# Kernel tuning notes

Measured on AMD Instinct MI355X. Metric: run time of the kernel, lower is better.

## Reference

```python
import jax, jax.numpy as jnp
import numpy as np

B, H, W, C = 2, 256, 256, 192
HEADS, WS, SHIFT = 6, 8, 4
N = WS * WS              # tokens per window = 64
NW = (H // WS) * (W // WS)  # windows per image = 1024
DH = C // HEADS
HID = 4 * C
EPS = 1e-5


def _rel_pos_index(ws):
    coords = np.stack(np.meshgrid(np.arange(ws), np.arange(ws), indexing='ij'))  # (2, ws, ws)
    flat = coords.reshape(2, -1)
    rel = flat[:, :, None] - flat[:, None, :]           # (2, N, N)
    rel = rel.transpose(1, 2, 0).astype(np.int64)       # (N, N, 2)
    rel[:, :, 0] += ws - 1
    rel[:, :, 1] += ws - 1
    rel[:, :, 0] *= 2 * ws - 1
    return rel.sum(-1).astype(np.int32)                 # (N, N)


def _attn_mask(h, w, ws, shift):
    img = np.zeros((h, w), np.float32)
    slc = (slice(0, -ws), slice(-ws, -shift), slice(-shift, None))
    cnt = 0
    for hs in slc:
        for wcol in slc:
            img[hs, wcol] = cnt
            cnt += 1
    mw = img.reshape(h // ws, ws, w // ws, ws).transpose(0, 2, 1, 3).reshape(-1, ws * ws)
    am = mw[:, None, :] - mw[:, :, None]
    return np.where(am != 0, np.float32(-100.0), np.float32(0.0)).astype(np.float32)


def setup_inputs() -> dict:
    key = jax.random.key(0)
    ks = jax.random.split(key, 8)
    s = 0.02
    return {
        'x': jax.random.normal(ks[0], (B, H * W, C), jnp.float32),
        'ln1_g': jnp.ones((C,), jnp.float32),
        'ln1_b': jnp.zeros((C,), jnp.float32),
        'qkv_w': jax.random.normal(ks[1], (3 * C, C), jnp.float32) * s,
        'qkv_b': jnp.zeros((3 * C,), jnp.float32),
        'rpb_table': jax.random.normal(ks[2], ((2 * WS - 1) ** 2, HEADS), jnp.float32) * s,
        'proj_w': jax.random.normal(ks[3], (C, C), jnp.float32) * s,
        'proj_b': jnp.zeros((C,), jnp.float32),
        'ln2_g': jnp.ones((C,), jnp.float32),
        'ln2_b': jnp.zeros((C,), jnp.float32),
        'fc1_w': jax.random.normal(ks[4], (HID, C), jnp.float32) * s,
        'fc1_b': jnp.zeros((HID,), jnp.float32),
        'fc2_w': jax.random.normal(ks[5], (C, HID), jnp.float32) * s,
        'fc2_b': jnp.zeros((C,), jnp.float32),
        'attn_mask': jnp.asarray(_attn_mask(H, W, WS, SHIFT)),   # (NW, N, N)
        'rel_idx': jnp.asarray(_rel_pos_index(WS)),               # (N, N) int32
    }


def _ln(x, g, b):
    m = jnp.mean(x, axis=-1, keepdims=True)
    v = jnp.mean(jnp.square(x - m), axis=-1, keepdims=True)
    return (x - m) * jax.lax.rsqrt(v + EPS) * g + b


def reference(x, ln1_g, ln1_b, qkv_w, qkv_b, rpb_table, proj_w, proj_b,
              ln2_g, ln2_b, fc1_w, fc1_b, fc2_w, fc2_b, attn_mask, rel_idx):
    nH, nW = H // WS, W // WS
    shortcut = x
    h = _ln(x, ln1_g, ln1_b).reshape(B, H, W, C)
    # cyclic shift
    h = jnp.roll(h, (-SHIFT, -SHIFT), axis=(1, 2))
    # window partition -> (B*NW, N, C)
    wins = h.reshape(B, nH, WS, nW, WS, C).transpose(0, 1, 3, 2, 4, 5).reshape(B * NW, N, C)
    qkv = wins @ qkv_w.T + qkv_b                       # (B*NW, N, 3C)
    qkv = qkv.reshape(B * NW, N, 3, HEADS, DH).transpose(2, 0, 3, 1, 4)
    q, k, v = qkv[0], qkv[1], qkv[2]                   # (B*NW, heads, N, DH)
    scale = DH ** -0.5
    attn = jnp.einsum('bhnd,bhmd->bhnm', q * scale, k)  # (B*NW, heads, N, N)
    bias = rpb_table[rel_idx.reshape(-1)].reshape(N, N, HEADS).transpose(2, 0, 1)
    attn = attn + bias[None]
    # shifted-window mask: per-window additive mask
    attn = attn.reshape(B, NW, HEADS, N, N) + attn_mask[None, :, None]
    attn = jax.nn.softmax(attn, axis=-1).reshape(B * NW, HEADS, N, N)
    out = jnp.einsum('bhnm,bhmd->bhnd', attn, v)        # (B*NW, heads, N, DH)
    out = out.transpose(0, 2, 1, 3).reshape(B * NW, N, C)
    out = out @ proj_w.T + proj_b
    # window reverse + unshift
    out = out.reshape(B, nH, nW, WS, WS, C).transpose(0, 1, 3, 2, 4, 5).reshape(B, H, W, C)
    out = jnp.roll(out, (SHIFT, SHIFT), axis=(1, 2)).reshape(B, H * W, C)
    x = shortcut + out
    h2 = _ln(x, ln2_g, ln2_b)
    h2 = jax.nn.gelu(h2 @ fc1_w.T + fc1_b, approximate=False)
    return x + (h2 @ fc2_w.T + fc2_b)
```

## Files before the change

kernel.cpp:

```cpp
#include <hip/hip_runtime.h>
#include <hip/hip_bf16.h>
#include <math.h>

using bf16 = __hip_bfloat16;
typedef short bfrag __attribute__((ext_vector_type(8)));
typedef float f32x4 __attribute__((ext_vector_type(4)));

__device__ __forceinline__ float b2f(bf16 v){ return __bfloat162float(v); }
__device__ __forceinline__ bf16  f2b(float v){ return __float2bfloat16(v); }
__device__ __forceinline__ short f2bs(float v){ bf16 t = f2b(v); union{bf16 h; short s;} u; u.h = t; return u.s; }
__device__ __forceinline__ float bits2f(unsigned short s){ union{unsigned u; float f;} c; c.u = ((unsigned)s) << 16; return c.f; }
__device__ __forceinline__ int   pk2(float lo, float hi){
  return (((int)(unsigned short)f2bs(hi)) << 16) | (int)(unsigned short)f2bs(lo);
}
__device__ __forceinline__ float ldT(const float* p, long long i){ return p[i]; }
__device__ __forceinline__ float ldT(const bf16*  p, long long i){ return __bfloat162float(p[i]); }

__device__ __forceinline__ bfrag ldfrag(const bf16* p){ return *reinterpret_cast<const bfrag*>(p); }
__device__ __forceinline__ f32x4 mm16(bfrag a, bfrag b, f32x4 c){
  return __builtin_amdgcn_mfma_f32_16x16x32_bf16(a, b, c, 0, 0, 0);
}
__device__ __forceinline__ void gload_lds16(const void* g, void* l){
  __builtin_amdgcn_global_load_lds(
    (const __attribute__((address_space(1))) unsigned int*)g,
    (__attribute__((address_space(3))) unsigned int*)l, 16, 0, 0);
}

template<int CTRL>
__device__ __forceinline__ float dppf(float v){
  union{float f; int i;} u; u.f = v;
  u.i = __builtin_amdgcn_update_dpp(0, u.i, CTRL, 0xF, 0xF, true);
  return u.f;
}
__device__ __forceinline__ float rmax16(float v){
  v = fmaxf(v, dppf<0xB1>(v));  v = fmaxf(v, dppf<0x4E>(v));
  v = fmaxf(v, dppf<0x141>(v)); v = fmaxf(v, dppf<0x140>(v));
  return v;
}
__device__ __forceinline__ float rsum16(float v){
  v += dppf<0xB1>(v);  v += dppf<0x4E>(v);
  v += dppf<0x141>(v); v += dppf<0x140>(v);
  return v;
}
__device__ __forceinline__ float rsum4(float v){
  v += dppf<0xB1>(v); v += dppf<0x4E>(v);
  return v;
}

__device__ __forceinline__ int reg1(int g){ return (g >= 248) + (g >= 252); }
__device__ __forceinline__ long long natidx(int gw, int t){
  const int wl = gw & 1023;
  const int sr = (((wl >> 5) << 3) + (t >> 3) + 4) & 255;
  const int sc = (((wl & 31) << 3) + (t & 7) + 4) & 255;
  return (((long long)(gw >> 10)) << 16) + sr*256 + sc;
}

template<typename T>
__device__ __forceinline__ void ld48(const T* p, long long off, float* d){
  if constexpr (sizeof(T) == 4){
    #pragma unroll
    for (int i = 0; i < 12; ++i){
      float4 v = *reinterpret_cast<const float4*>((const float*)p + off + i*4);
      d[i*4+0]=v.x; d[i*4+1]=v.y; d[i*4+2]=v.z; d[i*4+3]=v.w;
    }
  } else {
    #pragma unroll
    for (int i = 0; i < 6; ++i){
      bfrag v = *reinterpret_cast<const bfrag*>((const bf16*)p + off + i*8);
      #pragma unroll
      for (int j = 0; j < 8; ++j) d[i*8+j] = bits2f((unsigned short)v[j]);
    }
  }
}

#define WS_QKV   0
#define WS_PROJ  221184
#define WS_FC1   294912
#define WS_FC2   589824
#define WS_BIAS6 884736

__global__ __launch_bounds__(256) void prep_k(const void* det,
    const void* qkvw, const void* projw, const void* fc1w, const void* fc2w,
    const void* rpb, const int* __restrict__ relidx, char* wsb)
{
  const bool isbf = (((const unsigned short*)det)[0] == 0x3F80u);
  const int gt = blockIdx.x * 256 + threadIdx.x;
  if (gt < 55296) {
    const int fid = gt >> 6, l = gt & 63;
    int f, nkt, ckw; const void* src; bf16* dst;
    if (fid < 216)      { f = fid;       nkt = 6;  ckw = 192; src = qkvw;  dst = (bf16*)(wsb + WS_QKV); }
    else if (fid < 288) { f = fid - 216; nkt = 6;  ckw = 192; src = projw; dst = (bf16*)(wsb + WS_PROJ); }
    else if (fid < 576) { f = fid - 288; nkt = 6;  ckw = 192; src = fc1w;  dst = (bf16*)(wsb + WS_FC1); }
    else                { f = fid - 576; nkt = 24; ckw = 768; src = fc2w;  dst = (bf16*)(wsb + WS_FC2); }
    const int ct = f / nkt, kt = f - ct * nkt;
    const long long ro = (long long)(ct*16 + (l & 15)) * ckw + kt*32 + (l >> 4)*8;
    bf16* dp = dst + ((long long)f * 64 + l) * 8;
    #pragma unroll
    for (int j = 0; j < 8; ++j) {
      float v = isbf ? b2f(((const bf16*)src)[ro + j]) : ((const float*)src)[ro + j];
      dp[j] = f2b(v);
    }
  } else if (gt < 55296 + 24576) {
    const int t = gt - 55296;
    const int h = t >> 12, ij = t & 4095;
    const int ri = relidx[ij];
    float v = isbf ? b2f(((const bf16*)rpb)[ri*6 + h]) : ((const float*)rpb)[ri*6 + h];
    ((float*)(wsb + WS_BIAS6))[t] = v;
  }
}

#define XN_S 200
#define QK_S 72
#define VT_S 72
#define LDS_K1 (64*XN_S*2 + 64*QK_S*2 + 32*VT_S*2)

template<typename T>
__device__ void attn_body(const T* __restrict__ x, const T* __restrict__ g1, const T* __restrict__ b1,
                          const bf16* __restrict__ qkvwp, const T* __restrict__ qkvb,
                          const bf16* __restrict__ projwp, const T* __restrict__ projb,
                          const float* __restrict__ bias6, char* __restrict__ dout,
                          int x2f32, char* smem)
{
  bf16* xn = (bf16*)smem;
  bf16* qk = xn + 64*XN_S;
  bf16* vt = qk + 64*QK_S;
  const int tid = threadIdx.x, l = tid & 63, w = tid >> 6;
  const int lr = l & 15, lg = l >> 4;
  const int gw = blockIdx.x;
  const int wl = gw & 1023, wi = wl >> 5, wj = wl & 31;

  {
    const int t = (w << 4) + (l >> 2);
    const int c0 = (l & 3) * 48;
    const long long base = natidx(gw, t) * 192 + c0;
    float xv[48];
    ld48(x, base, xv);
    float s1 = 0.f, s2 = 0.f;
    #pragma unroll
    for (int i = 0; i < 48; ++i){ s1 += xv[i]; s2 = fmaf(xv[i], xv[i], s2); }
    s1 = rsum4(s1); s2 = rsum4(s2);
    const float m  = s1 * (1.f/192.f);
    const float rs = rsqrtf(s2*(1.f/192.f) - m*m + 1e-5f);
    bf16* xr = xn + t*XN_S + c0;
    #pragma unroll
    for (int cb = 0; cb < 6; ++cb){
      bfrag o;
      #pragma unroll
      for (int j = 0; j < 8; ++j){
        const int c = cb*8 + j;
        o[j] = f2bs((xv[c]-m)*rs*ldT(g1, c0+c) + ldT(b1, c0+c));
      }
      *reinterpret_cast<bfrag*>(xr + cb*8) = o;
    }
  }
  __syncthreads();

  int rjh[4], rjw[4], rih[4], riw[4];
  #pragma unroll
  for (int ct = 0; ct < 4; ++ct){
    const int j = ct*16 + lr;
    rjh[ct] = reg1(wi*8 + (j >> 3));
    rjw[ct] = reg1(wj*8 + (j & 7));
  }
  #pragma unroll
  for (int r = 0; r < 4; ++r){
    const int i = w*16 + lg*4 + r;
    rih[r] = reg1(wi*8 + (i >> 3));
    riw[r] = reg1(wj*8 + (i & 7));
  }

  int ohpk[6][2][2];

  #pragma unroll
  for (int h = 0; h < 6; ++h){
    f32x4 acc[6];
    #pragma unroll
    for (int u = 0; u < 6; ++u) acc[u] = (f32x4){0.f,0.f,0.f,0.f};
    #pragma unroll
    for (int kt = 0; kt < 6; ++kt){
      bfrag a = ldfrag(&xn[(w*16 + lr)*XN_S + kt*32 + lg*8]);
      bfrag bq[6];
      #pragma unroll
      for (int u = 0; u < 6; ++u){
        const int ctg = (u >> 1)*12 + 2*h + (u & 1);
        bq[u] = ldfrag(qkvwp + ((long long)(ctg*6 + kt)*64 + l)*8);
      }
      #pragma unroll
      for (int u = 0; u < 6; ++u) acc[u] = mm16(a, bq[u], acc[u]);
    }
    __syncthreads();

    #pragma unroll
    for (int u = 0; u < 6; ++u){
      const int ctg = (u >> 1)*12 + 2*h + (u & 1);
      const float bia = ldT(qkvb, ctg*16 + lr);
      #pragma unroll
      for (int r = 0; r < 4; ++r){
        const int row = w*16 + lg*4 + r;
        const float v = acc[u][r] + bia;
        if (u < 2)      qk[row*QK_S + u*16 + lr] = f2b(v * 0.17677669529663687f);
        else if (u < 4) qk[row*QK_S + 32 + (u & 1)*16 + lr] = f2b(v);
        else            vt[((u & 1)*16 + lr)*VT_S + row] = f2b(v);
      }
    }
    __syncthreads();

    f32x4 s4[4];
    {
      bfrag aq = ldfrag(&qk[(w*16 + lr)*QK_S + lg*8]);
      #pragma unroll
      for (int ct = 0; ct < 4; ++ct)
        s4[ct] = mm16(aq, ldfrag(&qk[(ct*16 + lr)*QK_S + 32 + lg*8]), (f32x4){0.f,0.f,0.f,0.f});
    }
    const float* bh = bias6 + h*4096;
    float pr[4][4], inv4[4];
    #pragma unroll
    for (int r = 0; r < 4; ++r){
      const int i = w*16 + lg*4 + r;
      const int ib = i*64 + lr;
      float v[4];
      #pragma unroll
      for (int ct = 0; ct < 4; ++ct){
        const float msk = (rih[r] == rjh[ct] && riw[r] == rjw[ct]) ? 0.f : -100.f;
        v[ct] = s4[ct][r] + bh[ib + ct*16] + msk;
      }
      float mx = rmax16(fmaxf(fmaxf(v[0],v[1]), fmaxf(v[2],v[3])));
      v[0] = __expf(v[0]-mx); v[1] = __expf(v[1]-mx);
      v[2] = __expf(v[2]-mx); v[3] = __expf(v[3]-mx);
      const float sm = rsum16(v[0]+v[1]+v[2]+v[3]);
      inv4[r] = __fdividef(1.f, sm);
      pr[r][0]=v[0]; pr[r][1]=v[1]; pr[r][2]=v[2]; pr[r][3]=v[3];
    }
    __syncthreads();

    #pragma unroll
    for (int r = 0; r < 4; ++r){
      const int i = w*16 + lg*4 + r;
      #pragma unroll
      for (int ct = 0; ct < 4; ++ct)
        qk[i*QK_S + ct*16 + lr] = f2b(pr[r][ct]*inv4[r]);
    }
    f32x4 o2[2] = {(f32x4){0.f,0.f,0.f,0.f}, (f32x4){0.f,0.f,0.f,0.f}};
    #pragma unroll
    for (int ktp = 0; ktp < 2; ++ktp){
      bfrag ap = ldfrag(&qk[(w*16 + lr)*QK_S + ktp*32 + lg*8]);
      o2[0] = mm16(ap, ldfrag(&vt[(lr)*VT_S + ktp*32 + lg*8]), o2[0]);
      o2[1] = mm16(ap, ldfrag(&vt[(16 + lr)*VT_S + ktp*32 + lg*8]), o2[1]);
    }
    #pragma unroll
    for (int u = 0; u < 2; ++u){
      ohpk[h][u][0] = pk2(o2[u][0], o2[u][1]);
      ohpk[h][u][1] = pk2(o2[u][2], o2[u][3]);
    }
  }

  #pragma unroll
  for (int h = 0; h < 6; ++h)
    #pragma unroll
    for (int u = 0; u < 2; ++u)
      #pragma unroll
      for (int rr = 0; rr < 2; ++rr){
        const int pk = ohpk[h][u][rr];
        const int row = w*16 + lg*4 + rr*2;
        *reinterpret_cast<short*>(&xn[row*XN_S + h*32 + u*16 + lr]) = (short)(pk & 0xffff);
        *reinterpret_cast<short*>(&xn[(row+1)*XN_S + h*32 + u*16 + lr]) = (short)(((unsigned)pk) >> 16);
      }
  __syncthreads();

  const int mp = w >> 1, chh = w & 1;
  f32x4 pacc[2][6];
  #pragma unroll
  for (int mt = 0; mt < 2; ++mt)
    #pragma unroll
    for (int cc = 0; cc < 6; ++cc) pacc[mt][cc] = (f32x4){0.f,0.f,0.f,0.f};
  #pragma unroll
  for (int kt = 0; kt < 6; ++kt){
    bfrag a0 = ldfrag(&xn[(mp*32 + lr)*XN_S + kt*32 + lg*8]);
    bfrag a1 = ldfrag(&xn[(mp*32 + 16 + lr)*XN_S + kt*32 + lg*8]);
    #pragma unroll
    for (int cc = 0; cc < 6; ++cc){
      bfrag bp = ldfrag(projwp + ((long long)((chh*6 + cc)*6 + kt)*64 + l)*8);
      pacc[0][cc] = mm16(a0, bp, pacc[0][cc]);
      pacc[1][cc] = mm16(a1, bp, pacc[1][cc]);
    }
  }
  #pragma unroll
  for (int mt = 0; mt < 2; ++mt)
    #pragma unroll
    for (int r = 0; r < 4; ++r){
      const int t = mp*32 + mt*16 + lg*4 + r;
      const long long n = natidx(gw, t);
      #pragma unroll
      for (int cc = 0; cc < 6; ++cc){
        const int c = (chh*6 + cc)*16 + lr;
        const float y = pacc[mt][cc][r] + ldT(projb, c) + ldT(x, n*192 + c);
        if (x2f32) ((float*)(dout + n*768))[c] = y;
        else       ((bf16*)(dout + n*384))[c]  = f2b(y);
      }
    }
}

__global__ __launch_bounds__(256, 4) void swin_attn_k(
    const void* det, const void* x, const void* g1, const void* b1,
    const bf16* qkvwp, const void* qkvb, const bf16* projwp, const void* projb,
    const float* bias6, void* doutv)
{
  extern __shared__ char smem[];
  const bool isbf = (((const unsigned short*)det)[0] == 0x3F80u);
  char* dout = (char*)doutv;
  if (isbf)
    attn_body<bf16>((const bf16*)x, (const bf16*)g1, (const bf16*)b1, qkvwp,
                    (const bf16*)qkvb, projwp, (const bf16*)projb, bias6, dout, 0, smem);
  else
    attn_body<float>((const float*)x, (const float*)g1, (const float*)b1, qkvwp,
                     (const float*)qkvb, projwp, (const float*)projb, bias6, dout, 1, smem);
}

#define HS_S 72
#define LDS_K3 (48*512*2 + 128*HS_S*2)

template<typename T>
__device__ void mlp_body(const T* __restrict__ g2, const T* __restrict__ b2,
                         const bf16* __restrict__ fc1p, const T* __restrict__ fb1,
                         const bf16* __restrict__ fc2p, const T* __restrict__ fb2,
                         char* __restrict__ dout, int outf32, char* smem)
{
  bf16* xn2 = (bf16*)smem;
  bf16* bw  = (bf16*)smem;
  bf16* hs  = bw + 48*512;
  const int tid = threadIdx.x, l = tid & 63, w = tid >> 6;
  const int lr = l & 15, lg = l >> 4;
  const long long t0 = (long long)blockIdx.x * 128;

  #pragma unroll
  for (int it = 0; it < 2; ++it){
    const int t = w*32 + it*16 + (l >> 2);
    const int c0 = (l & 3) * 48;
    const long long n = t0 + t;
    float xv[48];
    if (outf32) ld48((const float*)(dout + n*768), c0, xv);
    else        ld48((const bf16*)(dout + n*384), c0, xv);
    float s1 = 0.f, s2 = 0.f;
    #pragma unroll
    for (int i = 0; i < 48; ++i){ s1 += xv[i]; s2 = fmaf(xv[i], xv[i], s2); }
    s1 = rsum4(s1); s2 = rsum4(s2);
    const float m  = s1 * (1.f/192.f);
    const float rs = rsqrtf(s2*(1.f/192.f) - m*m + 1e-5f);
    bf16* xr = xn2 + t*XN_S + c0;
    #pragma unroll
    for (int cb = 0; cb < 6; ++cb){
      bfrag o;
      #pragma unroll
      for (int j = 0; j < 8; ++j){
        const int c = cb*8 + j;
        o[j] = f2bs((xv[c]-m)*rs*ldT(g2, c0+c) + ldT(b2, c0+c));
      }
      *reinterpret_cast<bfrag*>(xr + cb*8) = o;
    }
  }
  __syncthreads();

  bfrag xa[2][6];
  #pragma unroll
  for (int mt = 0; mt < 2; ++mt)
    #pragma unroll
    for (int kt = 0; kt < 6; ++kt)
      xa[mt][kt] = ldfrag(&xn2[(w*32 + mt*16 + lr)*XN_S + kt*32 + lg*8]);
  __syncthreads();

  f32x4 fa[2][12];
  #pragma unroll
  for (int mt = 0; mt < 2; ++mt)
    #pragma unroll
    for (int ct = 0; ct < 12; ++ct) fa[mt][ct] = (f32x4){0.f,0.f,0.f,0.f};

  for (int c = 0; c < 12; ++c){
    {
      const int q0 = w*12;
      #pragma unroll
      for (int e = 0; e < 12; ++e){
        const int q = q0 + e;
        const bf16* src = (q < 24)
          ? fc1p + ((long long)(c*24 + q)*64 + l)*8
          : fc2p + ((long long)(((q-24) >> 1)*24 + c*2 + ((q-24) & 1))*64 + l)*8;
        gload_lds16(src, bw + q*512);
      }
    }
    __syncthreads();
    f32x4 a1[2][4];
    #pragma unroll
    for (int mt = 0; mt < 2; ++mt)
      #pragma unroll
      for (int u = 0; u < 4; ++u) a1[mt][u] = (f32x4){0.f,0.f,0.f,0.f};
    #pragma unroll
    for (int kt = 0; kt < 6; ++kt)
      #pragma unroll
      for (int u = 0; u < 4; ++u){
        bfrag bq = ldfrag(&bw[((u*6 + kt)*64 + l)*8]);
        a1[0][u] = mm16(xa[0][kt], bq, a1[0][u]);
        a1[1][u] = mm16(xa[1][kt], bq, a1[1][u]);
      }
    #pragma unroll
    for (int u = 0; u < 4; ++u){
      const float bia = ldT(fb1, c*64 + u*16 + lr);
      #pragma unroll
      for (int mt = 0; mt < 2; ++mt)
        #pragma unroll
        for (int r = 0; r < 4; ++r){
          const float xv = a1[mt][u][r] + bia;
          const float g  = __fdividef(xv, 1.f + __expf(-1.702f*xv));
          hs[(w*32 + mt*16 + lg*4 + r)*HS_S + u*16 + lr] = f2b(g);
        }
    }
    #pragma unroll
    for (int ktl = 0; ktl < 2; ++ktl){
      bfrag aH0 = ldfrag(&hs[(w*32 + lr)*HS_S + ktl*32 + lg*8]);
      bfrag aH1 = ldfrag(&hs[(w*32 + 16 + lr)*HS_S + ktl*32 + lg*8]);
      #pragma unroll
      for (int ct = 0; ct < 12; ++ct){
        bfrag bq = ldfrag(&bw[((24 + ct*2 + ktl)*64 + l)*8]);
        fa[0][ct] = mm16(aH0, bq, fa[0][ct]);
        fa[1][ct] = mm16(aH1, bq, fa[1][ct]);
      }
    }
    __syncthreads();
  }

  #pragma unroll
  for (int mt = 0; mt < 2; ++mt)
    #pragma unroll
    for (int r = 0; r < 4; ++r){
      const long long n = t0 + w*32 + mt*16 + lg*4 + r;
      #pragma unroll
      for (int ct = 0; ct < 12; ++ct){
        const int cc = ct*16 + lr;
        float resid = outf32 ? ((const float*)(dout + n*768))[cc]
                             : b2f(((const bf16*)(dout + n*384))[cc]);
        const float y = fa[mt][ct][r] + ldT(fb2, cc) + resid;
        if (outf32) ((float*)(dout + n*768))[cc] = y;
        else        ((bf16*)(dout + n*384))[cc]  = f2b(y);
      }
    }
}

__global__ __launch_bounds__(256, 2) void swin_mlp_k(
    const void* det, const void* g2, const void* b2, const bf16* fc1p, const void* fb1,
    const bf16* fc2p, const void* fb2, void* doutv)
{
  extern __shared__ char smem[];
  const bool isbf = (((const unsigned short*)det)[0] == 0x3F80u);
  char* dout = (char*)doutv;
  if (isbf)
    mlp_body<bf16>((const bf16*)g2, (const bf16*)b2, fc1p, (const bf16*)fb1,
                   fc2p, (const bf16*)fb2, dout, 0, smem);
  else
    mlp_body<float>((const float*)g2, (const float*)b2, fc1p, (const float*)fb1,
                    fc2p, (const float*)fb2, dout, 1, smem);
}

extern "C" void kernel_launch(void* const* d_in, const int* in_sizes, int n_in,
                              void* d_out, int out_size, void* d_ws, size_t ws_size,
                              hipStream_t stream)
{
  (void)in_sizes; (void)n_in; (void)out_size; (void)ws_size;
  char* ws = (char*)d_ws;

  (void)hipFuncSetAttribute((const void*)swin_attn_k, hipFuncAttributeMaxDynamicSharedMemorySize, LDS_K1);
  (void)hipFuncSetAttribute((const void*)swin_mlp_k,  hipFuncAttributeMaxDynamicSharedMemorySize, LDS_K3);

  prep_k<<<dim3(312), dim3(256), 0, stream>>>(
      d_in[1], d_in[3], d_in[6], d_in[10], d_in[12], d_in[5], (const int*)d_in[15], ws);

  swin_attn_k<<<dim3(2048), dim3(256), LDS_K1, stream>>>(
      d_in[1], d_in[0], d_in[1], d_in[2],
      (const bf16*)(ws + WS_QKV), d_in[4], (const bf16*)(ws + WS_PROJ), d_in[7],
      (const float*)(ws + WS_BIAS6), d_out);

  swin_mlp_k<<<dim3(1024), dim3(256), LDS_K3, stream>>>(
      d_in[1], d_in[8], d_in[9],
      (const bf16*)(ws + WS_FC1), d_in[11], (const bf16*)(ws + WS_FC2), d_in[13], d_out);
}
```

Measured before the change: 313.2 us.

## Hoist LN activations to registers and software-pipeline per-head QKV GEMM

The normalized window activations are loaded once into registers instead of being reloaded from LDS for every head. The QKV projection for head h+1 is issued before head h's attention math, so the MFMA work overlaps the softmax and PV stages. The probability matrix now goes to the xn buffer, which frees it after the register hoist, and this drops one barrier per head. The shifted-window mask compare is folded into a single region id. In exchange the kernel holds more live registers (xa fragments plus the prefetched accumulators), which may lower occupancy.

Measured after the change: 317.6 us. Within noise of the previous version (+1.4%).

```diff
diff --git a/kernel.cpp b/kernel.cpp
--- a/kernel.cpp
+++ b/kernel.cpp
@@ -153,43 +153,44 @@
       *reinterpret_cast<bfrag*>(xr + cb*8) = o;
     }
   }
-  __syncthreads();
-
-  int rjh[4], rjw[4], rih[4], riw[4];
+
+  bfrag xa[6];
+  #pragma unroll
+  for (int kt = 0; kt < 6; ++kt)
+    xa[kt] = ldfrag(&xn[(w*16 + lr)*XN_S + kt*32 + lg*8]);
+
+  int cj[4], ci[4];
   #pragma unroll
   for (int ct = 0; ct < 4; ++ct){
     const int j = ct*16 + lr;
-    rjh[ct] = reg1(wi*8 + (j >> 3));
-    rjw[ct] = reg1(wj*8 + (j & 7));
+    cj[ct] = reg1(wi*8 + (j >> 3))*3 + reg1(wj*8 + (j & 7));
   }
   #pragma unroll
   for (int r = 0; r < 4; ++r){
     const int i = w*16 + lg*4 + r;
-    rih[r] = reg1(wi*8 + (i >> 3));
-    riw[r] = reg1(wj*8 + (i & 7));
+    ci[r] = reg1(wi*8 + (i >> 3))*3 + reg1(wj*8 + (i & 7));
   }
 
   int ohpk[6][2][2];
 
+  f32x4 acc[6];
+  #pragma unroll
+  for (int u = 0; u < 6; ++u) acc[u] = (f32x4){0.f,0.f,0.f,0.f};
+  #pragma unroll
+  for (int kt = 0; kt < 6; ++kt){
+    bfrag bq[6];
+    #pragma unroll
+    for (int u = 0; u < 6; ++u){
+      const int ctg = (u >> 1)*12 + (u & 1);
+      bq[u] = ldfrag(qkvwp + ((long long)(ctg*6 + kt)*64 + l)*8);
+    }
+    #pragma unroll
+    for (int u = 0; u < 6; ++u) acc[u] = mm16(xa[kt], bq[u], acc[u]);
+  }
+
   #pragma unroll
   for (int h = 0; h < 6; ++h){
-    f32x4 acc[6];
-    #pragma unroll
-    for (int u = 0; u < 6; ++u) acc[u] = (f32x4){0.f,0.f,0.f,0.f};
-    #pragma unroll
-    for (int kt = 0; kt < 6; ++kt){
-      bfrag a = ldfrag(&xn[(w*16 + lr)*XN_S + kt*32 + lg*8]);
-      bfrag bq[6];
-      #pragma unroll
-      for (int u = 0; u < 6; ++u){
-        const int ctg = (u >> 1)*12 + 2*h + (u & 1);
-        bq[u] = ldfrag(qkvwp + ((long long)(ctg*6 + kt)*64 + l)*8);
-      }
-      #pragma unroll
-      for (int u = 0; u < 6; ++u) acc[u] = mm16(a, bq[u], acc[u]);
-    }
     __syncthreads();
-
     #pragma unroll
     for (int u = 0; u < 6; ++u){
       const int ctg = (u >> 1)*12 + 2*h + (u & 1);
@@ -205,6 +206,22 @@
     }
     __syncthreads();
 
+    if (h < 5){
+      #pragma unroll
+      for (int u = 0; u < 6; ++u) acc[u] = (f32x4){0.f,0.f,0.f,0.f};
+      #pragma unroll
+      for (int kt = 0; kt < 6; ++kt){
+        bfrag bq[6];
+        #pragma unroll
+        for (int u = 0; u < 6; ++u){
+          const int ctg = (u >> 1)*12 + 2*(h+1) + (u & 1);
+          bq[u] = ldfrag(qkvwp + ((long long)(ctg*6 + kt)*64 + l)*8);
+        }
+        #pragma unroll
+        for (int u = 0; u < 6; ++u) acc[u] = mm16(xa[kt], bq[u], acc[u]);
+      }
+    }
+
     f32x4 s4[4];
     {
       bfrag aq = ldfrag(&qk[(w*16 + lr)*QK_S + lg*8]);
@@ -213,7 +230,6 @@
         s4[ct] = mm16(aq, ldfrag(&qk[(ct*16 + lr)*QK_S + 32 + lg*8]), (f32x4){0.f,0.f,0.f,0.f});
     }
     const float* bh = bias6 + h*4096;
-    float pr[4][4], inv4[4];
     #pragma unroll
     for (int r = 0; r < 4; ++r){
       const int i = w*16 + lg*4 + r;
@@ -221,29 +237,22 @@
       float v[4];
       #pragma unroll
       for (int ct = 0; ct < 4; ++ct){
-        const float msk = (rih[r] == rjh[ct] && riw[r] == rjw[ct]) ? 0.f : -100.f;
+        const float msk = (ci[r] == cj[ct]) ? 0.f : -100.f;
         v[ct] = s4[ct][r] + bh[ib + ct*16] + msk;
       }
       float mx = rmax16(fmaxf(fmaxf(v[0],v[1]), fmaxf(v[2],v[3])));
       v[0] = __expf(v[0]-mx); v[1] = __expf(v[1]-mx);
       v[2] = __expf(v[2]-mx); v[3] = __expf(v[3]-mx);
       const float sm = rsum16(v[0]+v[1]+v[2]+v[3]);
-      inv4[r] = __fdividef(1.f, sm);
-      pr[r][0]=v[0]; pr[r][1]=v[1]; pr[r][2]=v[2]; pr[r][3]=v[3];
-    }
-    __syncthreads();
-
-    #pragma unroll
-    for (int r = 0; r < 4; ++r){
-      const int i = w*16 + lg*4 + r;
+      const float inv = __fdividef(1.f, sm);
       #pragma unroll
       for (int ct = 0; ct < 4; ++ct)
-        qk[i*QK_S + ct*16 + lr] = f2b(pr[r][ct]*inv4[r]);
+        xn[i*XN_S + ct*16 + lr] = f2b(v[ct]*inv);
     }
     f32x4 o2[2] = {(f32x4){0.f,0.f,0.f,0.f}, (f32x4){0.f,0.f,0.f,0.f}};
     #pragma unroll
     for (int ktp = 0; ktp < 2; ++ktp){
-      bfrag ap = ldfrag(&qk[(w*16 + lr)*QK_S + ktp*32 + lg*8]);
+      bfrag ap = ldfrag(&xn[(w*16 + lr)*XN_S + ktp*32 + lg*8]);
       o2[0] = mm16(ap, ldfrag(&vt[(lr)*VT_S + ktp*32 + lg*8]), o2[0]);
       o2[1] = mm16(ap, ldfrag(&vt[(16 + lr)*VT_S + ktp*32 + lg*8]), o2[1]);
     }
```
